# Optimization experiments

Measured on AMD Instinct MI355X. Metric: run time of the kernel, lower is better.

## Reference

```python
import jax, jax.numpy as jnp
import numpy as np

# fixed geometry: N = B2D * H * W pixels
B2D, H, W = 32, 112, 112
NCLS, NSUB, DIM = 4, 2, 256
PROTO_MOM = 0.999
SK_ITERS, SK_EPS = 3, 0.05
LN_EPS = 1e-5


def layer_norm(x, gamma, beta):
    mu = jnp.mean(x, axis=-1, keepdims=True)
    var = jnp.var(x, axis=-1, keepdims=True)
    return (x - mu) * jax.lax.rsqrt(var + LN_EPS) * gamma + beta


def l2_normalize(x):
    return x / jnp.maximum(jnp.linalg.norm(x, axis=-1, keepdims=True), 1e-12)


def masked_sinkhorn(sim_c, mask):
    # sim_c: [N, M] cosine sims for one class; mask: [N] bool (pixels of this class)
    # Faithful to distributed_sinkhorn, restricted to masked rows.
    m = mask.astype(sim_c.dtype)
    L = jnp.exp(sim_c / SK_EPS).T * m[None, :]          # [M, N]
    Bn = jnp.sum(m)
    M = L.shape[0]
    L = L / jnp.maximum(jnp.sum(L), 1e-30)
    for _ in range(SK_ITERS):
        L = L / jnp.maximum(jnp.sum(L, axis=1, keepdims=True), 1e-30) / M
        col = jnp.sum(L, axis=0, keepdims=True)
        L = jnp.where(m[None, :] > 0, L / jnp.maximum(col, 1e-30) / jnp.maximum(Bn, 1.0), 0.0)
    L = (L * Bn).T                                       # [N, M]
    idx = jnp.argmax(L, axis=1)
    q = jax.nn.one_hot(idx, M, dtype=sim_c.dtype) * m[:, None]  # hard assignment
    return q, idx


def setup_inputs() -> dict:
    key = jax.random.key(0)
    ks = jax.random.split(key, 3)
    N = B2D * H * W
    return {
        "out_feat": jax.random.normal(ks[0], (N, DIM), dtype=jnp.float32),
        "label": jax.random.randint(ks[1], (N,), 0, NCLS, dtype=jnp.int64),
        "prototypes": jax.random.normal(ks[2], (NCLS, NSUB, DIM), dtype=jnp.float32),
        "fn_gamma": jnp.ones((DIM,), jnp.float32),
        "fn_beta": jnp.zeros((DIM,), jnp.float32),
        "mn_gamma": jnp.ones((NCLS,), jnp.float32),
        "mn_beta": jnp.zeros((NCLS,), jnp.float32),
    }


def reference(out_feat, label, prototypes, fn_gamma, fn_beta, mn_gamma, mn_beta):
    N = out_feat.shape[0]
    feat = l2_normalize(layer_norm(out_feat, fn_gamma, fn_beta))      # [N, D]
    protos = l2_normalize(prototypes)                                  # [K, M, D]
    sim = jnp.einsum('nd,kmd->nmk', feat, protos)                      # [N, M, K]
    nearest = layer_norm(jnp.max(sim, axis=1), mn_gamma, mn_beta)      # [N, K]
    pred = jnp.argmax(nearest, axis=-1)
    correct = (label == pred)                                          # [N] bool

    proto_logits = sim.reshape(N, NSUB * NCLS)
    proto_target = jnp.zeros((N,), jnp.float32)
    new_protos = protos
    for c in range(NCLS):
        cls_mask = (label == c)
        q, idx = masked_sinkhorn(sim[:, :, c], cls_mask)               # q:[N,M], masked
        mk = (cls_mask & correct).astype(feat.dtype)[:, None]
        m_q = q * mk                                                   # [N, M]
        f = m_q.T @ (feat * mk)                                        # [M, D]
        n = jnp.sum(m_q, axis=0)                                       # [M]
        f = l2_normalize(f)
        upd = PROTO_MOM * protos[c] + (1.0 - PROTO_MOM) * f
        upd = jnp.where(((jnp.sum(n) > 0) & (n != 0))[:, None], upd, protos[c])
        new_protos = new_protos.at[c].set(upd)
        proto_target = jnp.where(cls_mask, idx.astype(jnp.float32) + NSUB * c, proto_target)
    new_protos = l2_normalize(new_protos)

    nearest_img = nearest.reshape(B2D, H, W, NCLS).transpose(0, 3, 1, 2)  # [b, K, h, w]
    return nearest_img, proto_logits, proto_target, new_protos
```

## Files before the change

### kernel.cpp

```cpp
#include <hip/hip_runtime.h>
#include <stdint.h>

#define N_PIX 401408
#define HWIMG 12544
#define LN_EPS 1e-5f
#define NBLK 3136
#define ITERS 8

struct Ws {
  double R[3][8];
  unsigned cnt4[4];
  unsigned nmk[8];
  unsigned pad[4];
  float  protoN[8][256];
  float  fAcc[8][256];
  double   partR[NBLK][8];
  unsigned partC[NBLK][4];
  unsigned partNc[NBLK];
  unsigned char corrTmp[NBLK][128];
  float2 E2[N_PIX];
};

__device__ __forceinline__ float wredf(float v) {
#pragma unroll
  for (int o = 32; o > 0; o >>= 1) v += __shfl_xor(v, o, 64);
  return v;
}
__device__ __forceinline__ float wred16(float v) {
  v += __shfl_xor(v, 1, 64);
  v += __shfl_xor(v, 2, 64);
  v += __shfl_xor(v, 4, 64);
  v += __shfl_xor(v, 8, 64);
  return v;
}
__device__ __forceinline__ double wredd(double v) {
#pragma unroll
  for (int o = 32; o > 0; o >>= 1) v += __shfl_xor(v, o, 64);
  return v;
}
__device__ __forceinline__ unsigned wredu(unsigned v) {
#pragma unroll
  for (int o = 32; o > 0; o >>= 1) v += (unsigned)__shfl_xor((int)v, o, 64);
  return v;
}

__global__ __launch_bounds__(256) void k_main(
    const float* __restrict__ X, const int* __restrict__ label,
    const float* __restrict__ protos,
    const float* __restrict__ fng, const float* __restrict__ fnb,
    const float* __restrict__ mng, const float* __restrict__ mnb,
    Ws* __restrict__ ws,
    float* __restrict__ out_nearest, float* __restrict__ out_logits) {
  __shared__ float prS[2048];
  __shared__ double sRd[4][8];
  __shared__ unsigned sC4[4][4];
  __shared__ unsigned sCorr;
  __shared__ unsigned char sList[128];
  int tid = threadIdx.x;
  int wave = tid >> 6, lane = tid & 63;
  if (tid == 0) sCorr = 0u;

#pragma unroll
  for (int t = 0; t < 2; t++) {
    int r = wave + t * 4;
    const float4 p = *(const float4*)(protos + r * 256 + lane * 4);
    float ss = p.x * p.x + p.y * p.y + p.z * p.z + p.w * p.w;
    ss = wredf(ss);
    float inv = 1.0f / fmaxf(sqrtf(ss), 1e-12f);
    float4 o; o.x = p.x * inv; o.y = p.y * inv; o.z = p.z * inv; o.w = p.w * inv;
    *(float4*)(&prS[lane * 32 + 4 * (r ^ (lane & 7))]) = o;
    if (blockIdx.x == 0) *(float4*)(&ws->protoN[r][lane * 4]) = o;
  }
  __syncthreads();

  int grp = lane >> 4, s = lane & 15;

  const float* gb = fng + s * 4;
  const float* bb = fnb + s * 4;
  const float4 g0 = *(const float4*)(gb);
  const float4 g1 = *(const float4*)(gb + 64);
  const float4 g2 = *(const float4*)(gb + 128);
  const float4 g3 = *(const float4*)(gb + 192);
  const float4 b0 = *(const float4*)(bb);
  const float4 b1 = *(const float4*)(bb + 64);
  const float4 b2 = *(const float4*)(bb + 128);
  const float4 b3 = *(const float4*)(bb + 192);
  int k = (s >> 1) & 3;
  float mngk = mng[k], mnbk = mnb[k];

  double rAcc = 0.0;
  unsigned cAcc = 0u;

  for (int it = 0; it < ITERS; ++it) {
    int n = blockIdx.x * (16 * ITERS) + it * 16 + wave * 4 + grp;

    const float* xb = X + (size_t)n * 256 + s * 4;
    const float4 x0 = *(const float4*)(xb);
    const float4 x1 = *(const float4*)(xb + 64);
    const float4 x2 = *(const float4*)(xb + 128);
    const float4 x3 = *(const float4*)(xb + 192);
    int lab = label[n];

    float sm = (x0.x + x0.y + x0.z + x0.w) + (x1.x + x1.y + x1.z + x1.w) +
               (x2.x + x2.y + x2.z + x2.w) + (x3.x + x3.y + x3.z + x3.w);
    float q = x0.x * x0.x + x0.y * x0.y + x0.z * x0.z + x0.w * x0.w +
              x1.x * x1.x + x1.y * x1.y + x1.z * x1.z + x1.w * x1.w +
              x2.x * x2.x + x2.y * x2.y + x2.z * x2.z + x2.w * x2.w +
              x3.x * x3.x + x3.y * x3.y + x3.z * x3.z + x3.w * x3.w;
    sm = wred16(sm); q = wred16(q);
    float mu = sm * (1.0f / 256.0f);
    float var = q * (1.0f / 256.0f) - mu * mu;
    float rstd = rsqrtf(var + LN_EPS);

    float4 y0, y1, y2, y3;
    y0.x = (x0.x - mu) * rstd * g0.x + b0.x; y0.y = (x0.y - mu) * rstd * g0.y + b0.y;
    y0.z = (x0.z - mu) * rstd * g0.z + b0.z; y0.w = (x0.w - mu) * rstd * g0.w + b0.w;
    y1.x = (x1.x - mu) * rstd * g1.x + b1.x; y1.y = (x1.y - mu) * rstd * g1.y + b1.y;
    y1.z = (x1.z - mu) * rstd * g1.z + b1.z; y1.w = (x1.w - mu) * rstd * g1.w + b1.w;
    y2.x = (x2.x - mu) * rstd * g2.x + b2.x; y2.y = (x2.y - mu) * rstd * g2.y + b2.y;
    y2.z = (x2.z - mu) * rstd * g2.z + b2.z; y2.w = (x2.w - mu) * rstd * g2.w + b2.w;
    y3.x = (x3.x - mu) * rstd * g3.x + b3.x; y3.y = (x3.y - mu) * rstd * g3.y + b3.y;
    y3.z = (x3.z - mu) * rstd * g3.z + b3.z; y3.w = (x3.w - mu) * rstd * g3.w + b3.w;

    float qq = y0.x * y0.x + y0.y * y0.y + y0.z * y0.z + y0.w * y0.w +
               y1.x * y1.x + y1.y * y1.y + y1.z * y1.z + y1.w * y1.w +
               y2.x * y2.x + y2.y * y2.y + y2.z * y2.z + y2.w * y2.w +
               y3.x * y3.x + y3.y * y3.y + y3.z * y3.z + y3.w * y3.w;
    qq = wred16(qq);

    float dot[8];
#pragma unroll
    for (int j = 0; j < 8; j++) {
      int jx = 4 * (j ^ (s & 7));
      const float4 pa = *(const float4*)(&prS[s * 32 + jx]);
      const float4 pb = *(const float4*)(&prS[(16 + s) * 32 + jx]);
      const float4 pc = *(const float4*)(&prS[(32 + s) * 32 + jx]);
      const float4 pd = *(const float4*)(&prS[(48 + s) * 32 + jx]);
      dot[j] = y0.x * pa.x + y0.y * pa.y + y0.z * pa.z + y0.w * pa.w +
               y1.x * pb.x + y1.y * pb.y + y1.z * pb.z + y1.w * pb.w +
               y2.x * pc.x + y2.y * pc.y + y2.z * pc.z + y2.w * pc.w +
               y3.x * pd.x + y3.y * pd.y + y3.z * pd.z + y3.w * pd.w;
    }
    int b0s = s & 1, b1s = (s >> 1) & 1, b2s = (s >> 2) & 1;
    float e0 = b0s ? dot[1] : dot[0], o0 = b0s ? dot[0] : dot[1];
    float e1 = b0s ? dot[3] : dot[2], o1 = b0s ? dot[2] : dot[3];
    float e2 = b0s ? dot[5] : dot[4], o2 = b0s ? dot[4] : dot[5];
    float e3 = b0s ? dot[7] : dot[6], o3 = b0s ? dot[6] : dot[7];
    e0 += __shfl_xor(o0, 1, 64);
    e1 += __shfl_xor(o1, 1, 64);
    e2 += __shfl_xor(o2, 1, 64);
    e3 += __shfl_xor(o3, 1, 64);
    float f0 = b1s ? e1 : e0, p0 = b1s ? e0 : e1;
    float f1 = b1s ? e3 : e2, p1 = b1s ? e2 : e3;
    f0 += __shfl_xor(p0, 2, 64);
    f1 += __shfl_xor(p1, 2, 64);
    float h = b2s ? f1 : f0, ph = b2s ? f0 : f1;
    h += __shfl_xor(ph, 4, 64);
    float v = h + __shfl_xor(h, 8, 64);

    float invq = 1.0f / fmaxf(sqrtf(qq), 1e-12f);
    float d = v * invq;

    if (s < 8) out_logits[(size_t)n * 8 + ((s & 1) << 2) + (s >> 1)] = d;

    float nm = fmaxf(d, __shfl_xor(d, 1, 64));
    float tA = __shfl_xor(nm, 2, 64);
    float s2 = nm + tA, q2 = nm * nm + tA * tA;
    float s4 = s2 + __shfl_xor(s2, 4, 64);
    float q4 = q2 + __shfl_xor(q2, 4, 64);
    float m4 = 0.25f * s4;
    float v4 = 0.25f * q4 - m4 * m4;
    float rs4 = rsqrtf(v4 + LN_EPS);
    float lnv = (nm - m4) * rs4 * mngk + mnbk;

    int bimg = n / HWIMG;
    int p = n - bimg * HWIMG;
    if (s < 8 && (s & 1) == 0)
      out_nearest[((size_t)bimg * 4 + k) * HWIMG + p] = lnv;

    float av = lnv; int ak = k;
#pragma unroll
    for (int o = 2; o <= 4; o <<= 1) {
      float ov = __shfl_xor(av, o, 64);
      int ok = __shfl_xor(ak, o, 64);
      bool take = (ov > av) || (ov == av && ok < ak);
      av = take ? ov : av;
      ak = take ? ok : ak;
    }

    float Ev = expf(d / 0.05f);
    bool isLab = (s < 8) && ((s >> 1) == lab);
    if (isLab) ((float*)(ws->E2 + n))[s & 1] = Ev;
    float val = isLab ? Ev : 0.f;
    val += __shfl_xor(val, 16, 64);
    val += __shfl_xor(val, 32, 64);
    rAcc += (double)val;
    unsigned cu = ((s < 8) && !(s & 1) && ((s >> 1) == lab)) ? 1u : 0u;
    cu += (unsigned)__shfl_xor((int)cu, 16, 64);
    cu += (unsigned)__shfl_xor((int)cu, 32, 64);
    cAcc += cu;

    if (s == 0 && lab == ak) {
      unsigned pos = atomicAdd(&sCorr, 1u);
      sList[pos] = (unsigned char)(it * 16 + wave * 4 + grp);
    }
  }

  if (lane < 8) sRd[wave][lane] = rAcc;
  if (lane < 8 && !(lane & 1)) sC4[wave][lane >> 1] = cAcc;
  __syncthreads();
  if (tid < 8)
    ws->partR[blockIdx.x][tid] = sRd[0][tid] + sRd[1][tid] + sRd[2][tid] + sRd[3][tid];
  if (tid < 4)
    ws->partC[blockIdx.x][tid] = sC4[0][tid] + sC4[1][tid] + sC4[2][tid] + sC4[3][tid];
  unsigned nc = sCorr;
  if (tid == 0) ws->partNc[blockIdx.x] = nc;
  if (tid < (int)nc) ws->corrTmp[blockIdx.x][tid] = sList[tid];
}

__global__ __launch_bounds__(256) void k_red(Ws* __restrict__ ws) {
  __shared__ double ld[4];
  __shared__ unsigned lu[4];
  int b = blockIdx.x;
  int tid = threadIdx.x;
  int wave = tid >> 6, lane = tid & 63;
  if (b < 8) {
    double acc = 0.0;
    for (int r = tid; r < NBLK; r += 256) acc += ws->partR[r][b];
    acc = wredd(acc);
    if (lane == 0) ld[wave] = acc;
    __syncthreads();
    if (tid == 0) ws->R[0][b] = ld[0] + ld[1] + ld[2] + ld[3];
    if (b == 0) {
      if (tid < 16) ((double*)ws->R)[8 + tid] = 0.0;
      if (tid >= 16 && tid < 24) ws->nmk[tid - 16] = 0u;
    }
    if (b == 1) {
      for (int i = tid; i < 2048; i += 256) (&ws->fAcc[0][0])[i] = 0.f;
    }
  } else {
    int j = b - 8;
    unsigned acc = 0u;
    for (int r = tid; r < NBLK; r += 256) acc += ws->partC[r][j];
    acc = wredu(acc);
    if (lane == 0) lu[wave] = acc;
    __syncthreads();
    if (tid == 0) ws->cnt4[j] = lu[0] + lu[1] + lu[2] + lu[3];
  }
}

template <int ITER>
__global__ __launch_bounds__(256) void k_sink(const int* __restrict__ label,
                                              Ws* __restrict__ ws) {
  __shared__ float su1[8], su2[8], sBn[4];
  int tid = threadIdx.x;
  if (tid < 8) {
    int c = tid >> 1;
    float S = (float)ws->R[0][c * 2] + (float)ws->R[0][c * 2 + 1];
    float uu0 = 1.0f / fmaxf(S, 1e-30f);
    float R0 = (float)ws->R[0][tid];
    float uu1 = uu0 / (fmaxf(uu0 * R0, 1e-30f) * 2.0f);
    su1[tid] = uu1;
    if (ITER >= 3) {
      float R1 = (float)ws->R[1][tid];
      su2[tid] = uu1 / (fmaxf(uu1 * R1, 1e-30f) * 2.0f);
    }
  }
  if (tid < 4) sBn[tid] = fmaxf((float)ws->cnt4[tid], 1.0f);
  __syncthreads();

  double a0 = 0, a1 = 0, a2 = 0, a3 = 0, a4 = 0, a5 = 0, a6 = 0, a7 = 0;
  int gtid = blockIdx.x * 256 + tid;
  int T = gridDim.x * 256;
  for (int n = gtid; n < N_PIX; n += T) {
    int c = label[n];
    float2 e = ws->E2[n];
    float E0 = e.x, E1 = e.y;
    float S1 = su1[c * 2] * E0 + su1[c * 2 + 1] * E1;
    float v1 = 1.0f / (fmaxf(S1, 1e-30f) * sBn[c]);
    float v = v1;
    if (ITER >= 3) {
      float S2 = su2[c * 2] * E0 + su2[c * 2 + 1] * E1;
      v = v1 / (fmaxf(v1 * S2, 1e-30f) * sBn[c]);
    }
    double t0 = (double)(v * E0), t1 = (double)(v * E1);
    if (c == 0) { a0 += t0; a1 += t1; }
    else if (c == 1) { a2 += t0; a3 += t1; }
    else if (c == 2) { a4 += t0; a5 += t1; }
    else { a6 += t0; a7 += t1; }
  }
  a0 = wredd(a0); a1 = wredd(a1); a2 = wredd(a2); a3 = wredd(a3);
  a4 = wredd(a4); a5 = wredd(a5); a6 = wredd(a6); a7 = wredd(a7);
  __shared__ double lds[4][8];
  int wave = tid >> 6, lane = tid & 63;
  if (lane == 0) {
    lds[wave][0] = a0; lds[wave][1] = a1; lds[wave][2] = a2; lds[wave][3] = a3;
    lds[wave][4] = a4; lds[wave][5] = a5; lds[wave][6] = a6; lds[wave][7] = a7;
  }
  __syncthreads();
  if (tid < 8) {
    double ssum = lds[0][tid] + lds[1][tid] + lds[2][tid] + lds[3][tid];
    unsafeAtomicAdd(&ws->R[ITER - 1][tid], ssum);
  }
}

__global__ __launch_bounds__(256) void k_accum(
    const float* __restrict__ X, const int* __restrict__ label,
    const float* __restrict__ fng, const float* __restrict__ fnb,
    Ws* __restrict__ ws, float* __restrict__ out_target) {
  __shared__ float fa[4 * 2048];
  __shared__ float su[8];
  __shared__ unsigned ldc[4][8];
  int tid = threadIdx.x;
  if (tid < 8) {
    int c = tid >> 1;
    float S = (float)ws->R[0][c * 2] + (float)ws->R[0][c * 2 + 1];
    float uu0 = 1.0f / fmaxf(S, 1e-30f);
    float R0 = (float)ws->R[0][tid];
    float uu1 = uu0 / (fmaxf(uu0 * R0, 1e-30f) * 2.0f);
    float R1 = (float)ws->R[1][tid];
    float uu2 = uu1 / (fmaxf(uu1 * R1, 1e-30f) * 2.0f);
    float R2 = (float)ws->R[2][tid];
    su[tid] = uu2 / (fmaxf(uu2 * R2, 1e-30f) * 2.0f);
  }
  for (int i = tid; i < 4 * 2048; i += 256) fa[i] = 0.f;
  __syncthreads();

  int gtid = blockIdx.x * 256 + tid;
  int T = gridDim.x * 256;
  for (int n = gtid; n < N_PIX; n += T) {
    int c = label[n];
    float2 e = ws->E2[n];
    int idx = (su[c * 2 + 1] * e.y > su[c * 2] * e.x) ? 1 : 0;
    out_target[n] = (float)(idx + 2 * c);
  }

  int wave = tid >> 6, lane = tid & 63;
  const float4 g4 = *(const float4*)(fng + lane * 4);
  const float4 b4 = *(const float4*)(fnb + lane * 4);
  float* myAcc = &fa[wave * 2048];
  unsigned cl[8] = {0, 0, 0, 0, 0, 0, 0, 0};
  unsigned gw = blockIdx.x * 4 + wave;
  unsigned GW = gridDim.x * 4;
  for (unsigned b = gw; b < NBLK; b += GW) {
    unsigned cnt = ws->partNc[b];
    const unsigned char* lst = ws->corrTmp[b];
    for (unsigned base = 0; base < cnt; base += 4) {
      int m = (int)min(4u, cnt - base);
      int bk[4]; float4 xx[4];
#pragma unroll
      for (int g = 0; g < 4; g++) if (g < m) {
        int n = (int)(b * 128u) + (int)lst[base + g];
        int c = label[n];
        float2 e = ws->E2[n];
        int idx = (su[c * 2 + 1] * e.y > su[c * 2] * e.x) ? 1 : 0;
        bk[g] = c * 2 + idx;
        xx[g] = *(const float4*)(X + (size_t)n * 256 + lane * 4);
      }
      float svr[4], qvr[4];
#pragma unroll
      for (int g = 0; g < 4; g++) if (g < m) {
        float4 x = xx[g];
        float sv = x.x + x.y + x.z + x.w;
        float qv = x.x * x.x + x.y * x.y + x.z * x.z + x.w * x.w;
        svr[g] = wredf(sv); qvr[g] = wredf(qv);
      }
      float4 yy[4]; float qqr[4];
#pragma unroll
      for (int g = 0; g < 4; g++) if (g < m) {
        float mu = svr[g] * (1.0f / 256.0f);
        float var = qvr[g] * (1.0f / 256.0f) - mu * mu;
        float rstd = rsqrtf(var + LN_EPS);
        float4 x = xx[g];
        float4 y;
        y.x = (x.x - mu) * rstd * g4.x + b4.x;
        y.y = (x.y - mu) * rstd * g4.y + b4.y;
        y.z = (x.z - mu) * rstd * g4.z + b4.z;
        y.w = (x.w - mu) * rstd * g4.w + b4.w;
        yy[g] = y;
        qqr[g] = wredf(y.x * y.x + y.y * y.y + y.z * y.z + y.w * y.w);
      }
#pragma unroll
      for (int g = 0; g < 4; g++) if (g < m) {
        float invq = 1.0f / fmaxf(sqrtf(qqr[g]), 1e-12f);
        float4 y = yy[g];
        float* dst = myAcc + bk[g] * 256 + lane * 4;
        dst[0] += y.x * invq; dst[1] += y.y * invq;
        dst[2] += y.z * invq; dst[3] += y.w * invq;
        if (lane == 0) cl[bk[g]]++;
      }
    }
  }
  if (lane == 0) {
#pragma unroll
    for (int j = 0; j < 8; j++) ldc[wave][j] = cl[j];
  }
  __syncthreads();
  float* fg = &ws->fAcc[0][0];
  for (int i = tid; i < 2048; i += 256) {
    float ssum = fa[i] + fa[2048 + i] + fa[4096 + i] + fa[6144 + i];
    unsafeAtomicAdd(fg + i, ssum);
  }
  if (tid < 8) {
    unsigned cs = ldc[0][tid] + ldc[1][tid] + ldc[2][tid] + ldc[3][tid];
    if (cs) atomicAdd(&ws->nmk[tid], cs);
  }
}

__global__ __launch_bounds__(512) void k_final(Ws* __restrict__ ws, float* __restrict__ out_protos) {
  int tid = threadIdx.x;
  int r = tid >> 6, lane = tid & 63;
  const float4 f = *(const float4*)(&ws->fAcc[r][lane * 4]);
  float ss = wredf(f.x * f.x + f.y * f.y + f.z * f.z + f.w * f.w);
  float invf = 1.0f / fmaxf(sqrtf(ss), 1e-12f);
  unsigned nr = ws->nmk[r];
  int c = r >> 1;
  unsigned tot = ws->nmk[c * 2] + ws->nmk[c * 2 + 1];
  bool cond = (tot > 0u) && (nr != 0u);
  const float4 p = *(const float4*)(&ws->protoN[r][lane * 4]);
  float u0 = cond ? 0.999f * p.x + 0.001f * (f.x * invf) : p.x;
  float u1 = cond ? 0.999f * p.y + 0.001f * (f.y * invf) : p.y;
  float u2 = cond ? 0.999f * p.z + 0.001f * (f.z * invf) : p.z;
  float u3 = cond ? 0.999f * p.w + 0.001f * (f.w * invf) : p.w;
  float ss2 = wredf(u0 * u0 + u1 * u1 + u2 * u2 + u3 * u3);
  float invn = 1.0f / fmaxf(sqrtf(ss2), 1e-12f);
  float4 o; o.x = u0 * invn; o.y = u1 * invn; o.z = u2 * invn; o.w = u3 * invn;
  *(float4*)(out_protos + r * 256 + lane * 4) = o;
}

extern "C" void kernel_launch(void* const* d_in, const int* in_sizes, int n_in,
                              void* d_out, int out_size, void* d_ws, size_t ws_size,
                              hipStream_t stream) {
  const float* X = (const float*)d_in[0];
  const int* label = (const int*)d_in[1];
  const float* protos = (const float*)d_in[2];
  const float* fng = (const float*)d_in[3];
  const float* fnb = (const float*)d_in[4];
  const float* mng = (const float*)d_in[5];
  const float* mnb = (const float*)d_in[6];

  float* out = (float*)d_out;
  float* out_nearest = out;
  float* out_logits = out + 1605632;
  float* out_target = out_logits + 3211264;
  float* out_protos = out_target + N_PIX;
  Ws* ws = (Ws*)d_ws;

  k_main<<<NBLK, 256, 0, stream>>>(X, label, protos, fng, fnb, mng, mnb, ws, out_nearest, out_logits);
  k_red<<<12, 256, 0, stream>>>(ws);
  k_sink<2><<<512, 256, 0, stream>>>(label, ws);
  k_sink<3><<<512, 256, 0, stream>>>(label, ws);
  k_accum<<<512, 256, 0, stream>>>(X, label, fng, fnb, ws, out_target);
  k_final<<<1, 512, 0, stream>>>(ws, out_protos);
}
```

Measured before the change: 721.0 us.

## Fuse all stages into one cooperative persistent kernel with grid syncs

Replaces the six-kernel pipeline (main pass, partial reduction, two Sinkhorn passes, accumulation, final update) with one cooperative kernel. Stages are separated by grid.sync, and each block re-reduces the per-block partials itself instead of relying on a separate reduce kernel and global atomics on shared totals. The grid is sized from occupancy and blocks loop persistently over pixel chunks. Each block then accumulates prototype features for the correct pixels it found itself, into 8 partitioned accumulators to spread atomic contention. The aim is to remove launch gaps and tail effects between stages. In exchange it adds grid-wide barrier costs, redundant per-block reductions, and depends on every block being co-resident.

Result: slower. 1.268 ms (+75.9%).

```diff
diff --git a/kernel.cpp b/kernel.cpp
--- a/kernel.cpp
+++ b/kernel.cpp
@@ -1,24 +1,24 @@
 #include <hip/hip_runtime.h>
+#include <hip/hip_cooperative_groups.h>
 #include <stdint.h>
 
+namespace cg = cooperative_groups;
+
 #define N_PIX 401408
+#define NCHUNK 25088
 #define HWIMG 12544
 #define LN_EPS 1e-5f
-#define NBLK 3136
-#define ITERS 8
+#define MAXG 1024
 
 struct Ws {
-  double R[3][8];
-  unsigned cnt4[4];
-  unsigned nmk[8];
-  unsigned pad[4];
-  float  protoN[8][256];
-  float  fAcc[8][256];
-  double   partR[NBLK][8];
-  unsigned partC[NBLK][4];
-  unsigned partNc[NBLK];
-  unsigned char corrTmp[NBLK][128];
-  float2 E2[N_PIX];
+  double   partRa[MAXG][8];
+  double   partRb[MAXG][8];
+  double   partRc[MAXG][8];
+  unsigned partC[MAXG][4];
+  float    protoN[8][256];
+  float    fAccP[8][2048];
+  unsigned nmkP[8][8];
+  float2   E2[N_PIX];
 };
 
 __device__ __forceinline__ float wredf(float v) {
@@ -38,28 +38,54 @@
   for (int o = 32; o > 0; o >>= 1) v += __shfl_xor(v, o, 64);
   return v;
 }
-__device__ __forceinline__ unsigned wredu(unsigned v) {
-#pragma unroll
-  for (int o = 32; o > 0; o >>= 1) v += (unsigned)__shfl_xor((int)v, o, 64);
-  return v;
-}
-
-__global__ __launch_bounds__(256) void k_main(
+
+__device__ __forceinline__ void red8(const double (*part)[8], int G, int tid,
+                                     double* sRed, float* Rf) {
+  int j = tid & 7;
+  double acc = 0.0;
+  for (int i = tid >> 3; i < G; i += 32) acc += part[i][j];
+  sRed[tid] = acc;
+  __syncthreads();
+  if (tid < 8) {
+    double t = 0.0;
+#pragma unroll
+    for (int r2 = 0; r2 < 32; r2++) t += sRed[tid + r2 * 8];
+    Rf[tid] = (float)t;
+  }
+  __syncthreads();
+}
+
+__global__ __launch_bounds__(256, 4) void k_all(
     const float* __restrict__ X, const int* __restrict__ label,
     const float* __restrict__ protos,
     const float* __restrict__ fng, const float* __restrict__ fnb,
     const float* __restrict__ mng, const float* __restrict__ mnb,
     Ws* __restrict__ ws,
-    float* __restrict__ out_nearest, float* __restrict__ out_logits) {
-  __shared__ float prS[2048];
+    float* __restrict__ out_nearest, float* __restrict__ out_logits,
+    float* __restrict__ out_target, float* __restrict__ out_protos) {
+  cg::grid_group grid = cg::this_grid();
+
+  __shared__ float bigS[8192];
+  __shared__ double sRed[256];
+  __shared__ float Rf[8], su1[8], su2[8], su3[8], sBn[4];
+  __shared__ unsigned short sList[800];
+  __shared__ unsigned sCorr;
   __shared__ double sRd[4][8];
   __shared__ unsigned sC4[4][4];
-  __shared__ unsigned sCorr;
-  __shared__ unsigned char sList[128];
-  int tid = threadIdx.x;
-  int wave = tid >> 6, lane = tid & 63;
+  __shared__ unsigned ldc[4][8];
+
+  const int tid = threadIdx.x;
+  const int bid = blockIdx.x;
+  const int G = gridDim.x;
+  const int wave = tid >> 6, lane = tid & 63;
   if (tid == 0) sCorr = 0u;
 
+  if (bid < 8) {
+    for (int i = tid; i < 2048; i += 256) ws->fAccP[bid][i] = 0.f;
+    if (tid < 8) ws->nmkP[bid][tid] = 0u;
+  }
+
+  float* prS = bigS;
 #pragma unroll
   for (int t = 0; t < 2; t++) {
     int r = wave + t * 4;
@@ -69,12 +95,11 @@
     float inv = 1.0f / fmaxf(sqrtf(ss), 1e-12f);
     float4 o; o.x = p.x * inv; o.y = p.y * inv; o.z = p.z * inv; o.w = p.w * inv;
     *(float4*)(&prS[lane * 32 + 4 * (r ^ (lane & 7))]) = o;
-    if (blockIdx.x == 0) *(float4*)(&ws->protoN[r][lane * 4]) = o;
-  }
-  __syncthreads();
-
-  int grp = lane >> 4, s = lane & 15;
-
+    if (bid == 0) *(float4*)(&ws->protoN[r][lane * 4]) = o;
+  }
+  __syncthreads();
+
+  const int grp = lane >> 4, s = lane & 15;
   const float* gb = fng + s * 4;
   const float* bb = fnb + s * 4;
   const float4 g0 = *(const float4*)(gb);
@@ -85,14 +110,15 @@
   const float4 b1 = *(const float4*)(bb + 64);
   const float4 b2 = *(const float4*)(bb + 128);
   const float4 b3 = *(const float4*)(bb + 192);
-  int k = (s >> 1) & 3;
-  float mngk = mng[k], mnbk = mnb[k];
+  const int k = (s >> 1) & 3;
+  const float mngk = mng[k], mnbk = mnb[k];
 
   double rAcc = 0.0;
   unsigned cAcc = 0u;
 
-  for (int it = 0; it < ITERS; ++it) {
-    int n = blockIdx.x * (16 * ITERS) + it * 16 + wave * 4 + grp;
+  int it = 0;
+  for (int ch = bid; ch < NCHUNK; ch += G, ++it) {
+    int n = ch * 16 + wave * 4 + grp;
 
     const float* xb = X + (size_t)n * 256 + s * 4;
     const float4 x0 = *(const float4*)(xb);
@@ -202,7 +228,7 @@
 
     if (s == 0 && lab == ak) {
       unsigned pos = atomicAdd(&sCorr, 1u);
-      sList[pos] = (unsigned char)(it * 16 + wave * 4 + grp);
+      sList[pos] = (unsigned short)(it * 16 + wave * 4 + grp);
     }
   }
 
@@ -210,150 +236,128 @@
   if (lane < 8 && !(lane & 1)) sC4[wave][lane >> 1] = cAcc;
   __syncthreads();
   if (tid < 8)
-    ws->partR[blockIdx.x][tid] = sRd[0][tid] + sRd[1][tid] + sRd[2][tid] + sRd[3][tid];
+    ws->partRa[bid][tid] = sRd[0][tid] + sRd[1][tid] + sRd[2][tid] + sRd[3][tid];
   if (tid < 4)
-    ws->partC[blockIdx.x][tid] = sC4[0][tid] + sC4[1][tid] + sC4[2][tid] + sC4[3][tid];
-  unsigned nc = sCorr;
-  if (tid == 0) ws->partNc[blockIdx.x] = nc;
-  if (tid < (int)nc) ws->corrTmp[blockIdx.x][tid] = sList[tid];
-}
-
-__global__ __launch_bounds__(256) void k_red(Ws* __restrict__ ws) {
-  __shared__ double ld[4];
-  __shared__ unsigned lu[4];
-  int b = blockIdx.x;
-  int tid = threadIdx.x;
-  int wave = tid >> 6, lane = tid & 63;
-  if (b < 8) {
-    double acc = 0.0;
-    for (int r = tid; r < NBLK; r += 256) acc += ws->partR[r][b];
-    acc = wredd(acc);
-    if (lane == 0) ld[wave] = acc;
-    __syncthreads();
-    if (tid == 0) ws->R[0][b] = ld[0] + ld[1] + ld[2] + ld[3];
-    if (b == 0) {
-      if (tid < 16) ((double*)ws->R)[8 + tid] = 0.0;
-      if (tid >= 16 && tid < 24) ws->nmk[tid - 16] = 0u;
-    }
-    if (b == 1) {
-      for (int i = tid; i < 2048; i += 256) (&ws->fAcc[0][0])[i] = 0.f;
-    }
-  } else {
-    int j = b - 8;
-    unsigned acc = 0u;
-    for (int r = tid; r < NBLK; r += 256) acc += ws->partC[r][j];
-    acc = wredu(acc);
-    if (lane == 0) lu[wave] = acc;
-    __syncthreads();
-    if (tid == 0) ws->cnt4[j] = lu[0] + lu[1] + lu[2] + lu[3];
-  }
-}
-
-template <int ITER>
-__global__ __launch_bounds__(256) void k_sink(const int* __restrict__ label,
-                                              Ws* __restrict__ ws) {
-  __shared__ float su1[8], su2[8], sBn[4];
-  int tid = threadIdx.x;
+    ws->partC[bid][tid] = sC4[0][tid] + sC4[1][tid] + sC4[2][tid] + sC4[3][tid];
+
+  grid.sync();
+
+  red8(ws->partRa, G, tid, sRed, Rf);
   if (tid < 8) {
     int c = tid >> 1;
-    float S = (float)ws->R[0][c * 2] + (float)ws->R[0][c * 2 + 1];
+    float S = Rf[c * 2] + Rf[c * 2 + 1];
     float uu0 = 1.0f / fmaxf(S, 1e-30f);
-    float R0 = (float)ws->R[0][tid];
-    float uu1 = uu0 / (fmaxf(uu0 * R0, 1e-30f) * 2.0f);
-    su1[tid] = uu1;
-    if (ITER >= 3) {
-      float R1 = (float)ws->R[1][tid];
-      su2[tid] = uu1 / (fmaxf(uu1 * R1, 1e-30f) * 2.0f);
-    }
-  }
-  if (tid < 4) sBn[tid] = fmaxf((float)ws->cnt4[tid], 1.0f);
-  __syncthreads();
-
-  double a0 = 0, a1 = 0, a2 = 0, a3 = 0, a4 = 0, a5 = 0, a6 = 0, a7 = 0;
-  int gtid = blockIdx.x * 256 + tid;
-  int T = gridDim.x * 256;
-  for (int n = gtid; n < N_PIX; n += T) {
-    int c = label[n];
-    float2 e = ws->E2[n];
-    float E0 = e.x, E1 = e.y;
-    float S1 = su1[c * 2] * E0 + su1[c * 2 + 1] * E1;
-    float v1 = 1.0f / (fmaxf(S1, 1e-30f) * sBn[c]);
-    float v = v1;
-    if (ITER >= 3) {
-      float S2 = su2[c * 2] * E0 + su2[c * 2 + 1] * E1;
-      v = v1 / (fmaxf(v1 * S2, 1e-30f) * sBn[c]);
-    }
-    double t0 = (double)(v * E0), t1 = (double)(v * E1);
-    if (c == 0) { a0 += t0; a1 += t1; }
-    else if (c == 1) { a2 += t0; a3 += t1; }
-    else if (c == 2) { a4 += t0; a5 += t1; }
-    else { a6 += t0; a7 += t1; }
-  }
-  a0 = wredd(a0); a1 = wredd(a1); a2 = wredd(a2); a3 = wredd(a3);
-  a4 = wredd(a4); a5 = wredd(a5); a6 = wredd(a6); a7 = wredd(a7);
-  __shared__ double lds[4][8];
-  int wave = tid >> 6, lane = tid & 63;
-  if (lane == 0) {
-    lds[wave][0] = a0; lds[wave][1] = a1; lds[wave][2] = a2; lds[wave][3] = a3;
-    lds[wave][4] = a4; lds[wave][5] = a5; lds[wave][6] = a6; lds[wave][7] = a7;
-  }
-  __syncthreads();
-  if (tid < 8) {
-    double ssum = lds[0][tid] + lds[1][tid] + lds[2][tid] + lds[3][tid];
-    unsafeAtomicAdd(&ws->R[ITER - 1][tid], ssum);
-  }
-}
-
-__global__ __launch_bounds__(256) void k_accum(
-    const float* __restrict__ X, const int* __restrict__ label,
-    const float* __restrict__ fng, const float* __restrict__ fnb,
-    Ws* __restrict__ ws, float* __restrict__ out_target) {
-  __shared__ float fa[4 * 2048];
-  __shared__ float su[8];
-  __shared__ unsigned ldc[4][8];
-  int tid = threadIdx.x;
-  if (tid < 8) {
-    int c = tid >> 1;
-    float S = (float)ws->R[0][c * 2] + (float)ws->R[0][c * 2 + 1];
-    float uu0 = 1.0f / fmaxf(S, 1e-30f);
-    float R0 = (float)ws->R[0][tid];
-    float uu1 = uu0 / (fmaxf(uu0 * R0, 1e-30f) * 2.0f);
-    float R1 = (float)ws->R[1][tid];
-    float uu2 = uu1 / (fmaxf(uu1 * R1, 1e-30f) * 2.0f);
-    float R2 = (float)ws->R[2][tid];
-    su[tid] = uu2 / (fmaxf(uu2 * R2, 1e-30f) * 2.0f);
-  }
-  for (int i = tid; i < 4 * 2048; i += 256) fa[i] = 0.f;
-  __syncthreads();
-
-  int gtid = blockIdx.x * 256 + tid;
-  int T = gridDim.x * 256;
-  for (int n = gtid; n < N_PIX; n += T) {
-    int c = label[n];
-    float2 e = ws->E2[n];
-    int idx = (su[c * 2 + 1] * e.y > su[c * 2] * e.x) ? 1 : 0;
-    out_target[n] = (float)(idx + 2 * c);
-  }
-
-  int wave = tid >> 6, lane = tid & 63;
-  const float4 g4 = *(const float4*)(fng + lane * 4);
-  const float4 b4 = *(const float4*)(fnb + lane * 4);
-  float* myAcc = &fa[wave * 2048];
-  unsigned cl[8] = {0, 0, 0, 0, 0, 0, 0, 0};
-  unsigned gw = blockIdx.x * 4 + wave;
-  unsigned GW = gridDim.x * 4;
-  for (unsigned b = gw; b < NBLK; b += GW) {
-    unsigned cnt = ws->partNc[b];
-    const unsigned char* lst = ws->corrTmp[b];
-    for (unsigned base = 0; base < cnt; base += 4) {
-      int m = (int)min(4u, cnt - base);
+    su1[tid] = uu0 / (fmaxf(uu0 * Rf[tid], 1e-30f) * 2.0f);
+  }
+  {
+    unsigned* sRu = (unsigned*)sRed;
+    int c4 = tid & 3;
+    unsigned ua = 0;
+    for (int i = tid >> 2; i < G; i += 64) ua += ws->partC[i][c4];
+    __syncthreads();
+    sRu[tid] = ua;
+    __syncthreads();
+    if (tid < 4) {
+      unsigned t = 0;
+#pragma unroll
+      for (int r2 = 0; r2 < 64; r2++) t += sRu[tid + r2 * 4];
+      sBn[tid] = fmaxf((float)t, 1.0f);
+    }
+    __syncthreads();
+  }
+
+  {
+    double a0 = 0, a1 = 0, a2 = 0, a3 = 0, a4 = 0, a5 = 0, a6 = 0, a7 = 0;
+    int T = G * 256;
+    for (int n = bid * 256 + tid; n < N_PIX; n += T) {
+      int c = label[n];
+      float2 e = ws->E2[n];
+      float S1 = su1[c * 2] * e.x + su1[c * 2 + 1] * e.y;
+      float v1 = 1.0f / (fmaxf(S1, 1e-30f) * sBn[c]);
+      double t0 = (double)(v1 * e.x), t1 = (double)(v1 * e.y);
+      if (c == 0) { a0 += t0; a1 += t1; }
+      else if (c == 1) { a2 += t0; a3 += t1; }
+      else if (c == 2) { a4 += t0; a5 += t1; }
+      else { a6 += t0; a7 += t1; }
+    }
+    a0 = wredd(a0); a1 = wredd(a1); a2 = wredd(a2); a3 = wredd(a3);
+    a4 = wredd(a4); a5 = wredd(a5); a6 = wredd(a6); a7 = wredd(a7);
+    if (lane == 0) {
+      sRd[wave][0] = a0; sRd[wave][1] = a1; sRd[wave][2] = a2; sRd[wave][3] = a3;
+      sRd[wave][4] = a4; sRd[wave][5] = a5; sRd[wave][6] = a6; sRd[wave][7] = a7;
+    }
+    __syncthreads();
+    if (tid < 8)
+      ws->partRb[bid][tid] = sRd[0][tid] + sRd[1][tid] + sRd[2][tid] + sRd[3][tid];
+  }
+
+  grid.sync();
+
+  red8(ws->partRb, G, tid, sRed, Rf);
+  if (tid < 8)
+    su2[tid] = su1[tid] / (fmaxf(su1[tid] * Rf[tid], 1e-30f) * 2.0f);
+  __syncthreads();
+
+  {
+    double a0 = 0, a1 = 0, a2 = 0, a3 = 0, a4 = 0, a5 = 0, a6 = 0, a7 = 0;
+    int T = G * 256;
+    for (int n = bid * 256 + tid; n < N_PIX; n += T) {
+      int c = label[n];
+      float2 e = ws->E2[n];
+      float S1 = su1[c * 2] * e.x + su1[c * 2 + 1] * e.y;
+      float v1 = 1.0f / (fmaxf(S1, 1e-30f) * sBn[c]);
+      float S2 = su2[c * 2] * e.x + su2[c * 2 + 1] * e.y;
+      float v = v1 / (fmaxf(v1 * S2, 1e-30f) * sBn[c]);
+      double t0 = (double)(v * e.x), t1 = (double)(v * e.y);
+      if (c == 0) { a0 += t0; a1 += t1; }
+      else if (c == 1) { a2 += t0; a3 += t1; }
+      else if (c == 2) { a4 += t0; a5 += t1; }
+      else { a6 += t0; a7 += t1; }
+    }
+    a0 = wredd(a0); a1 = wredd(a1); a2 = wredd(a2); a3 = wredd(a3);
+    a4 = wredd(a4); a5 = wredd(a5); a6 = wredd(a6); a7 = wredd(a7);
+    if (lane == 0) {
+      sRd[wave][0] = a0; sRd[wave][1] = a1; sRd[wave][2] = a2; sRd[wave][3] = a3;
+      sRd[wave][4] = a4; sRd[wave][5] = a5; sRd[wave][6] = a6; sRd[wave][7] = a7;
+    }
+    __syncthreads();
+    if (tid < 8)
+      ws->partRc[bid][tid] = sRd[0][tid] + sRd[1][tid] + sRd[2][tid] + sRd[3][tid];
+  }
+
+  grid.sync();
+
+  red8(ws->partRc, G, tid, sRed, Rf);
+  if (tid < 8)
+    su3[tid] = su2[tid] / (fmaxf(su2[tid] * Rf[tid], 1e-30f) * 2.0f);
+  __syncthreads();
+
+  {
+    int T = G * 256;
+    for (int n = bid * 256 + tid; n < N_PIX; n += T) {
+      int c = label[n];
+      float2 e = ws->E2[n];
+      int idx = (su3[c * 2 + 1] * e.y > su3[c * 2] * e.x) ? 1 : 0;
+      out_target[n] = (float)(idx + 2 * c);
+    }
+
+    float* myAcc = &bigS[wave * 2048];
+    for (int i = lane; i < 2048; i += 64) myAcc[i] = 0.f;
+
+    const float4 g4 = *(const float4*)(fng + lane * 4);
+    const float4 b4 = *(const float4*)(fnb + lane * 4);
+    unsigned cl[8] = {0, 0, 0, 0, 0, 0, 0, 0};
+    unsigned nc = sCorr;
+    for (unsigned base = wave * 4; base < nc; base += 16) {
+      int m = (int)min(4u, nc - base);
       int bk[4]; float4 xx[4];
 #pragma unroll
       for (int g = 0; g < 4; g++) if (g < m) {
-        int n = (int)(b * 128u) + (int)lst[base + g];
+        int lid = sList[base + g];
+        int n = (bid + (lid >> 4) * G) * 16 + (lid & 15);
         int c = label[n];
         float2 e = ws->E2[n];
-        int idx = (su[c * 2 + 1] * e.y > su[c * 2] * e.x) ? 1 : 0;
+        int idx = (su3[c * 2 + 1] * e.y > su3[c * 2] * e.x) ? 1 : 0;
         bk[g] = c * 2 + idx;
         xx[g] = *(const float4*)(X + (size_t)n * 256 + lane * 4);
       }
@@ -390,42 +394,49 @@
         if (lane == 0) cl[bk[g]]++;
       }
     }
-  }
-  if (lane == 0) {
-#pragma unroll
-    for (int j = 0; j < 8; j++) ldc[wave][j] = cl[j];
-  }
-  __syncthreads();
-  float* fg = &ws->fAcc[0][0];
-  for (int i = tid; i < 2048; i += 256) {
-    float ssum = fa[i] + fa[2048 + i] + fa[4096 + i] + fa[6144 + i];
-    unsafeAtomicAdd(fg + i, ssum);
-  }
-  if (tid < 8) {
-    unsigned cs = ldc[0][tid] + ldc[1][tid] + ldc[2][tid] + ldc[3][tid];
-    if (cs) atomicAdd(&ws->nmk[tid], cs);
-  }
-}
-
-__global__ __launch_bounds__(512) void k_final(Ws* __restrict__ ws, float* __restrict__ out_protos) {
-  int tid = threadIdx.x;
-  int r = tid >> 6, lane = tid & 63;
-  const float4 f = *(const float4*)(&ws->fAcc[r][lane * 4]);
-  float ss = wredf(f.x * f.x + f.y * f.y + f.z * f.z + f.w * f.w);
-  float invf = 1.0f / fmaxf(sqrtf(ss), 1e-12f);
-  unsigned nr = ws->nmk[r];
-  int c = r >> 1;
-  unsigned tot = ws->nmk[c * 2] + ws->nmk[c * 2 + 1];
-  bool cond = (tot > 0u) && (nr != 0u);
-  const float4 p = *(const float4*)(&ws->protoN[r][lane * 4]);
-  float u0 = cond ? 0.999f * p.x + 0.001f * (f.x * invf) : p.x;
-  float u1 = cond ? 0.999f * p.y + 0.001f * (f.y * invf) : p.y;
-  float u2 = cond ? 0.999f * p.z + 0.001f * (f.z * invf) : p.z;
-  float u3 = cond ? 0.999f * p.w + 0.001f * (f.w * invf) : p.w;
-  float ss2 = wredf(u0 * u0 + u1 * u1 + u2 * u2 + u3 * u3);
-  float invn = 1.0f / fmaxf(sqrtf(ss2), 1e-12f);
-  float4 o; o.x = u0 * invn; o.y = u1 * invn; o.z = u2 * invn; o.w = u3 * invn;
-  *(float4*)(out_protos + r * 256 + lane * 4) = o;
+    if (lane == 0) {
+#pragma unroll
+      for (int j = 0; j < 8; j++) ldc[wave][j] = cl[j];
+    }
+    __syncthreads();
+    float* fg = &ws->fAccP[bid & 7][0];
+    for (int i = tid; i < 2048; i += 256) {
+      float ssum = bigS[i] + bigS[2048 + i] + bigS[4096 + i] + bigS[6144 + i];
+      unsafeAtomicAdd(fg + i, ssum);
+    }
+    if (tid < 8) {
+      unsigned cs = ldc[0][tid] + ldc[1][tid] + ldc[2][tid] + ldc[3][tid];
+      if (cs) atomicAdd(&ws->nmkP[bid & 7][tid], cs);
+    }
+  }
+
+  grid.sync();
+
+  if (bid < 8 && wave == 0) {
+    int r = bid;
+    float4 f = {0.f, 0.f, 0.f, 0.f};
+#pragma unroll
+    for (int p = 0; p < 8; p++) {
+      const float4 t = *(const float4*)(&ws->fAccP[p][r * 256 + lane * 4]);
+      f.x += t.x; f.y += t.y; f.z += t.z; f.w += t.w;
+    }
+    unsigned nr = 0, nsib = 0;
+#pragma unroll
+    for (int p = 0; p < 8; p++) { nr += ws->nmkP[p][r]; nsib += ws->nmkP[p][r ^ 1]; }
+    float ss = wredf(f.x * f.x + f.y * f.y + f.z * f.z + f.w * f.w);
+    float invf = 1.0f / fmaxf(sqrtf(ss), 1e-12f);
+    unsigned tot = nr + nsib;
+    bool cond = (tot > 0u) && (nr != 0u);
+    const float4 p4 = *(const float4*)(&ws->protoN[r][lane * 4]);
+    float u0 = cond ? 0.999f * p4.x + 0.001f * (f.x * invf) : p4.x;
+    float u1 = cond ? 0.999f * p4.y + 0.001f * (f.y * invf) : p4.y;
+    float u2 = cond ? 0.999f * p4.z + 0.001f * (f.z * invf) : p4.z;
+    float u3 = cond ? 0.999f * p4.w + 0.001f * (f.w * invf) : p4.w;
+    float ss2 = wredf(u0 * u0 + u1 * u1 + u2 * u2 + u3 * u3);
+    float invn = 1.0f / fmaxf(sqrtf(ss2), 1e-12f);
+    float4 o; o.x = u0 * invn; o.y = u1 * invn; o.z = u2 * invn; o.w = u3 * invn;
+    *(float4*)(out_protos + r * 256 + lane * 4) = o;
+  }
 }
 
 extern "C" void kernel_launch(void* const* d_in, const int* in_sizes, int n_in,
@@ -446,10 +457,15 @@
   float* out_protos = out_target + N_PIX;
   Ws* ws = (Ws*)d_ws;
 
-  k_main<<<NBLK, 256, 0, stream>>>(X, label, protos, fng, fnb, mng, mnb, ws, out_nearest, out_logits);
-  k_red<<<12, 256, 0, stream>>>(ws);
-  k_sink<2><<<512, 256, 0, stream>>>(label, ws);
-  k_sink<3><<<512, 256, 0, stream>>>(label, ws);
-  k_accum<<<512, 256, 0, stream>>>(X, label, fng, fnb, ws, out_target);
-  k_final<<<1, 512, 0, stream>>>(ws, out_protos);
-}
+  int occ = 0;
+  hipOccupancyMaxActiveBlocksPerMultiprocessor(&occ, k_all, 256, 0);
+  int G = occ * 256;
+  if (G < 512) G = 512;
+  if (G > MAXG) G = MAXG;
+
+  void* args[] = {(void*)&X, (void*)&label, (void*)&protos,
+                  (void*)&fng, (void*)&fnb, (void*)&mng, (void*)&mnb,
+                  (void*)&ws, (void*)&out_nearest, (void*)&out_logits,
+                  (void*)&out_target, (void*)&out_protos};
+  hipLaunchCooperativeKernel((void*)k_all, dim3(G), dim3(256), args, 0, stream);
+}
```
